# Optimization experiments

Measured on AMD Instinct MI355X. Metric: run time of the kernel, lower is better.

Reference implementation:

```python
import jax, jax.numpy as jnp
import numpy as np

K = 5        # spline kernel_size per dim (dim=2 -> 25 kernel weights)
NPG = 75     # MNIST superpixel nodes per graph


def _spline_conv(x, src, dst, pseudo, emask, W, root, bias):
    """SplineConv, dim=2, kernel_size=5, degree=1 open splines, aggr='mean'.
    emask in {0,1} masks out coalesced-away (duplicate/self-loop) edges."""
    n = x.shape[0]
    v = jnp.clip(pseudo, 0.0, 1.0) * (K - 1)
    bot = jnp.clip(jnp.floor(v), 0, K - 2)
    frac = v - bot                                   # [E,2]
    bot = bot.astype(jnp.int32)
    xj = x[src] * emask[:, None]                     # [E,Fin] gathered source feats
    # aggregate-then-transform: acc[k,i,:] = sum over edges into i with basis k
    acc = jnp.zeros((K * K, n, x.shape[1]), x.dtype)
    for o0 in (0, 1):
        for o1 in (0, 1):
            w = (frac[:, 0] if o0 else 1.0 - frac[:, 0]) * (frac[:, 1] if o1 else 1.0 - frac[:, 1])
            kk = (bot[:, 0] + o0) + K * (bot[:, 1] + o1)
            acc = acc.at[kk, dst].add(w[:, None] * xj)
    out = jnp.einsum('knf,kfo->no', acc, W)
    deg = jax.ops.segment_sum(emask, dst, num_segments=n)
    return out / jnp.maximum(deg, 1.0)[:, None] + x @ root + bias


def _pool(x, pos, valid, batch, src, dst, emask, size, G, B):
    """voxel_grid + max_pool with static shapes: S=B*G*G clusters, masked."""
    S = B * G * G
    c = jnp.clip(jnp.floor(pos / size).astype(jnp.int32), 0, G - 1)
    cl = batch * (G * G) + c[:, 1] * G + c[:, 0]
    xm = jnp.where(valid[:, None] > 0, x, -1e30)
    px = jax.ops.segment_max(xm, cl, num_segments=S)
    cnt = jax.ops.segment_sum(valid, cl, num_segments=S)
    sval = (cnt > 0).astype(x.dtype)
    px = jnp.where(sval[:, None] > 0, px, 0.0)
    ppos = jax.ops.segment_sum(pos * valid[:, None], cl, num_segments=S) / jnp.maximum(cnt, 1.0)[:, None]
    nb = jnp.arange(S, dtype=jnp.int32) // (G * G)
    # remap edges to clusters; mask self loops and duplicates (= coalesce)
    nsrc, ndst = cl[src], cl[dst]
    m = (emask > 0) & (nsrc != ndst)
    a0 = jnp.where(m, nsrc, S)
    b0 = jnp.where(m, ndst, S)
    order = jnp.lexsort((b0, a0))
    a, b = a0[order], b0[order]
    first = jnp.concatenate([jnp.array([True]), (a[1:] != a[:-1]) | (b[1:] != b[:-1])])
    keep = jnp.zeros(src.shape[0], dtype=bool).at[order].set(first & (a < S))
    kf = keep.astype(x.dtype)
    # T.Cartesian(cat=False, norm=True): pseudo = (pos_src-pos_dst)/(2*max|.|)+0.5
    cart = ppos[nsrc] - ppos[ndst]
    amax = jnp.maximum(jnp.max(jnp.abs(cart) * kf[:, None]), 1e-12)
    pseudo = cart / (2.0 * amax) + 0.5
    return px, ppos, sval, nb, nsrc, ndst, kf, pseudo


def _forward(x, pos, src, dst, W1, r1, b1, W2, r2, b2, W3, r3, b3, fw1, fb1, fw2, fb2):
    N = x.shape[0]
    B = N // NPG
    batch = jnp.arange(N, dtype=jnp.int32) // NPG
    valid = jnp.ones((N,), x.dtype)
    emask = jnp.ones((src.shape[0],), x.dtype)
    cart = pos[src] - pos[dst]
    pseudo = cart / (2.0 * jnp.maximum(jnp.max(jnp.abs(cart)), 1e-12)) + 0.5
    x = jax.nn.elu(_spline_conv(x, src, dst, pseudo, emask, W1, r1, b1))
    x, pos, valid, batch, src, dst, emask, pseudo = _pool(x, pos, valid, batch, src, dst, emask, 5.0, 6, B)
    x = jax.nn.elu(_spline_conv(x, src, dst, pseudo, emask, W2, r2, b2))
    x, pos, valid, batch, src, dst, emask, pseudo = _pool(x, pos, valid, batch, src, dst, emask, 7.0, 5, B)
    x = jax.nn.elu(_spline_conv(x, src, dst, pseudo, emask, W3, r3, b3))
    # max_pool_x(cluster, x, batch, size=4): 2x2 voxel grid (size=14, end=27.99)
    c = jnp.clip(jnp.floor(pos / 14.0).astype(jnp.int32), 0, 1)
    cl = batch * 4 + c[:, 1] * 2 + c[:, 0]
    xm = jnp.where(valid[:, None] > 0, x, -1e30)
    px = jax.ops.segment_max(xm, cl, num_segments=B * 4)
    cnt = jax.ops.segment_sum(valid, cl, num_segments=B * 4)
    px = jnp.where((cnt > 0)[:, None], px, 0.0)
    h = jax.nn.elu(px.reshape(B, 4 * 64) @ fw1.T + fb1)
    logits = h @ fw2.T + fb2  # F.dropout is identity in eval mode
    return jax.nn.log_softmax(logits, axis=1)


def setup_inputs() -> dict:
    key = jax.random.key(0)
    ks = jax.random.split(key, 16)
    B, EPG = 1024, 1392
    N = B * NPG
    x = jax.random.normal(ks[0], (N, 1), jnp.float32)
    pos = jax.random.uniform(ks[1], (N, 2), jnp.float32) * 27.99
    s = jax.random.randint(ks[2], (B, EPG), 0, NPG)
    d = (s + 1 + jax.random.randint(ks[3], (B, EPG), 0, NPG - 1)) % NPG  # no self loops
    off = (jnp.arange(B, dtype=jnp.int32) * NPG)[:, None]
    src = (s + off).reshape(-1)
    dst = (d + off).reshape(-1)
    rn = lambda k, sh, sc: jax.random.normal(k, sh, jnp.float32) * sc
    return dict(x=x, pos=pos, src=src, dst=dst,
                W1=rn(ks[4], (25, 1, 32), 0.2), r1=rn(ks[5], (1, 32), 0.2), b1=jnp.zeros((32,), jnp.float32),
                W2=rn(ks[6], (25, 32, 64), 0.05), r2=rn(ks[7], (32, 64), 0.1), b2=jnp.zeros((64,), jnp.float32),
                W3=rn(ks[8], (25, 64, 64), 0.04), r3=rn(ks[9], (64, 64), 0.08), b3=jnp.zeros((64,), jnp.float32),
                fw1=rn(ks[10], (128, 256), 0.06), fb1=jnp.zeros((128,), jnp.float32),
                fw2=rn(ks[11], (10, 128), 0.09), fb2=jnp.zeros((10,), jnp.float32))


def reference(x, pos, src, dst, W1, r1, b1, W2, r2, b2, W3, r3, b3, fw1, fb1, fw2, fb2):
    return _forward(x, pos, src, dst, W1, r1, b1, W2, r2, b2, W3, r3, b3, fw1, fb1, fw2, fb2)
```

## Files before the change

### kernel.cpp

```cpp
#include <hip/hip_runtime.h>
#include <math.h>

#define NPG 75
#define KDIM 5

typedef _Float16 half8 __attribute__((ext_vector_type(8)));
typedef _Float16 half4 __attribute__((ext_vector_type(4)));
typedef float f32x4 __attribute__((ext_vector_type(4)));

__device__ __forceinline__ float eluf(float v){ return v > 0.f ? v : expf(v) - 1.f; }

__device__ __forceinline__ void atomAddF(float* p, float v){ unsafeAtomicAdd(p, v); }

__device__ __forceinline__ unsigned fenc(float f){
    unsigned u = __float_as_uint(f);
    return (u & 0x80000000u) ? ~u : (u | 0x80000000u);
}
__device__ __forceinline__ float fdec(unsigned u){
    return (u & 0x80000000u) ? __uint_as_float(u & 0x7FFFFFFFu) : __uint_as_float(~u);
}

__device__ __forceinline__ void fma25(float (&r)[25], const float (&wx)[5], const float (&wyx)[5]){
    #pragma unroll
    for (int b1 = 0; b1 < 5; b1++)
        #pragma unroll
        for (int b0 = 0; b0 < 5; b0++)
            asm("v_fmac_f32 %0, %1, %2" : "+v"(r[b1 * 5 + b0]) : "v"(wx[b0]), "v"(wyx[b1]));
}

__device__ __forceinline__ void spline2(float c0, float c1, float am, int* kks, float* wsp){
    float denom = 2.f * fmaxf(am, 1e-12f);
    float p0 = c0 / denom + 0.5f;
    float p1 = c1 / denom + 0.5f;
    p0 = fminf(fmaxf(p0, 0.f), 1.f) * 4.f;
    p1 = fminf(fmaxf(p1, 0.f), 1.f) * 4.f;
    float b0 = fminf(floorf(p0), 3.f);
    float b1 = fminf(floorf(p1), 3.f);
    float f0 = p0 - b0, f1 = p1 - b1;
    int i0 = (int)b0, i1 = (int)b1;
    wsp[0] = (1.f - f0) * (1.f - f1); kks[0] = i0     + KDIM *  i1;
    wsp[1] =        f0  * (1.f - f1); kks[1] = i0 + 1 + KDIM *  i1;
    wsp[2] = (1.f - f0) *        f1 ; kks[2] = i0     + KDIM * (i1 + 1);
    wsp[3] =        f0  *        f1 ; kks[3] = i0 + 1 + KDIM * (i1 + 1);
}

__global__ __launch_bounds__(256) void amax0_k(
        const float* __restrict__ pos, const int* __restrict__ src,
        const int* __restrict__ dst, int E4, unsigned* __restrict__ outbits){
    float cand = 0.f;
    for (int i = blockIdx.x * 256 + threadIdx.x; i < E4; i += gridDim.x * 256){
        int4 s4 = ((const int4*)src)[i];
        int4 d4 = ((const int4*)dst)[i];
        #pragma unroll
        for (int k = 0; k < 4; k++){
            int s = (&s4.x)[k], d = (&d4.x)[k];
            float c0 = pos[s*2]   - pos[d*2];
            float c1 = pos[s*2+1] - pos[d*2+1];
            cand = fmaxf(cand, fmaxf(fabsf(c0), fabsf(c1)));
        }
    }
    __shared__ float sm[256];
    sm[threadIdx.x] = cand; __syncthreads();
    for (int o = 128; o > 0; o >>= 1){
        if (threadIdx.x < o) sm[threadIdx.x] = fmaxf(sm[threadIdx.x], sm[threadIdx.x + o]);
        __syncthreads();
    }
    if (threadIdx.x == 0) atomicMax(outbits, __float_as_uint(sm[0]));
}

__global__ __launch_bounds__(512) void conv1pool1_k(
        const float* __restrict__ x, const float* __restrict__ pos,
        const int* __restrict__ src, const int* __restrict__ dst, int EPG,
        const unsigned* __restrict__ amaxp,
        const float* __restrict__ W1, const float* __restrict__ r1, const float* __restrict__ b1,
        float* __restrict__ px1, float* __restrict__ pp1, float* __restrict__ sv1,
        int* __restrict__ cl1){
    __shared__ __align__(16) float acc[NPG * 28];
    __shared__ float deg[NPG];
    __shared__ float xl[NPG], p0l[NPG], p1l[NPG];
    __shared__ int   cli[NPG];
    __shared__ float W1s[800], r1s[32], b1s[32];
    __shared__ unsigned px[36 * 32];
    __shared__ float cnt[36], ps[72];

    const int b = blockIdx.x, t = threadIdx.x;
    const int n0 = b * NPG, e0 = b * EPG;

    const float am = __uint_as_float(*amaxp);

    for (int i = t; i < NPG * 28; i += 512) acc[i] = 0.f;
    for (int i = t; i < 36 * 32; i += 512) px[i] = 0u;
    if (t < NPG) deg[t] = 0.f;
    if (t < 36) cnt[t] = 0.f;
    if (t < 72) ps[t] = 0.f;
    for (int i = t; i < 800; i += 512) W1s[i] = W1[i];
    if (t < 32){ r1s[t] = r1[t]; b1s[t] = b1[t]; }
    if (t < NPG){
        float p0 = pos[(n0 + t) * 2], p1 = pos[(n0 + t) * 2 + 1];
        xl[t] = x[n0 + t]; p0l[t] = p0; p1l[t] = p1;
        int c0 = min(max((int)floorf(p0 / 5.f), 0), 5);
        int c1 = min(max((int)floorf(p1 / 5.f), 0), 5);
        int c = c1 * 6 + c0;
        cli[t] = c;
        cl1[n0 + t] = b * 36 + c;
    }
    __syncthreads();

    const int o = t & 31;
    float wreg[25];
    #pragma unroll
    for (int k = 0; k < 25; k++) wreg[k] = W1s[k * 32 + o];
    const float rro = r1s[o], bbo = b1s[o];

    if (t < NPG){
        int c = cli[t];
        atomAddF(&cnt[c], 1.f);
        atomAddF(&ps[c*2],     p0l[t]);
        atomAddF(&ps[c*2 + 1], p1l[t]);
    }

    for (int e = t; e < EPG; e += 512){
        int s = src[e0 + e] - n0;
        int d = dst[e0 + e] - n0;
        float c0 = p0l[s] - p0l[d];
        float c1 = p1l[s] - p1l[d];
        int kks[4]; float wsp[4];
        spline2(c0, c1, am, kks, wsp);
        float xv = xl[s];
        #pragma unroll
        for (int c = 0; c < 4; c++) atomAddF(&acc[d*28 + kks[c]], wsp[c] * xv);
        atomAddF(&deg[d], 1.f);
    }
    __syncthreads();

    const int ii = t >> 5;
    #pragma unroll
    for (int r = 0; r < 5; r++){
        int i = ii + r * 16;
        if (i < NPG){
            const float4* ar = (const float4*)(acc + i * 28);
            float s = 0.f;
            #pragma unroll
            for (int q = 0; q < 7; q++){
                float4 aq = ar[q];
                s += aq.x * wreg[q*4];
                if (q*4 + 1 < 25) s += aq.y * wreg[q*4 + 1];
                if (q*4 + 2 < 25) s += aq.z * wreg[q*4 + 2];
                if (q*4 + 3 < 25) s += aq.w * wreg[q*4 + 3];
            }
            float v = s / fmaxf(deg[i], 1.f) + xl[i] * rro + bbo;
            v = eluf(v);
            atomicMax(&px[cli[i]*32 + o], fenc(v));
        }
    }
    __syncthreads();

    for (int idx = t; idx < 36 * 32; idx += 512){
        int s_ = idx >> 5;
        px1[(size_t)(b*36)*32 + idx] = (cnt[s_] > 0.f) ? fdec(px[idx]) : 0.f;
    }
    if (t < 36){
        float c = cnt[t], m = fmaxf(c, 1.f);
        pp1[(b*36 + t)*2]     = ps[t*2] / m;
        pp1[(b*36 + t)*2 + 1] = ps[t*2 + 1] / m;
        sv1[b*36 + t] = (c > 0.f) ? 1.f : 0.f;
    }
}

template<int GG, int NN>
__global__ __launch_bounds__(1024) void dedup_csr_k(
        const int* src_in, const int* dst_in,
        const int* __restrict__ clmap, const unsigned char* __restrict__ kf_in,
        unsigned char* kf_out, int* es_out, int* ed_out,
        const float* __restrict__ pp, int EPG,
        int* __restrict__ easrc, float2* __restrict__ ecart,
        int* __restrict__ rowptr2, int* __restrict__ kcnt, unsigned* __restrict__ amaxbits){
    __shared__ unsigned pm[GG * GG];
    __shared__ float degs[GG];
    __shared__ int rs[GG + 1];
    __shared__ int cur[GG];
    __shared__ float red[16];
    __shared__ int   clS[NN];
    __shared__ float ppS[2 * GG];

    const int b = blockIdx.x, t = threadIdx.x;
    const int lane = t & 63, wid = t >> 6;
    const int e0 = b * EPG;
    const int cbase = b * GG;

    for (int i = t; i < GG * GG; i += 1024) pm[i] = 0xFFFFFFFFu;
    if (t < GG) degs[t] = 0.f;
    if (t < NN) clS[t] = clmap[b * NN + t] - cbase;
    if (t < 2 * GG) ppS[t] = pp[cbase * 2 + t];
    __syncthreads();

    const int niter = (EPG + 1023) / 1024;
    int la[2], lb[2]; bool lm[2];
    const int nbase = b * NN;
    for (int it = 0; it < niter; it++){
        int e = t + it * 1024;
        lm[it] = false;
        if (e < EPG){
            int a  = clS[src_in[e0 + e] - nbase];
            int bb = clS[dst_in[e0 + e] - nbase];
            la[it] = a; lb[it] = bb;
            es_out[e0 + e] = cbase + a; ed_out[e0 + e] = cbase + bb;
            bool m = (kf_in ? (kf_in[e0 + e] != 0) : true) && (a != bb);
            lm[it] = m;
            if (m) atomicMin(&pm[a * GG + bb], (unsigned)e);
        }
    }
    __syncthreads();

    float cand = 0.f;
    bool kept[2]; float lc0[2], lc1[2];
    for (int it = 0; it < niter; it++){
        int e = t + it * 1024;
        kept[it] = false;
        if (e < EPG){
            bool k = false;
            if (lm[it]) k = (pm[la[it] * GG + lb[it]] == (unsigned)e);
            kept[it] = k;
            if (kf_out) kf_out[e0 + e] = k ? 1 : 0;
            if (k){
                atomAddF(&degs[lb[it]], 1.f);
                float c0 = ppS[la[it]*2]     - ppS[lb[it]*2];
                float c1 = ppS[la[it]*2 + 1] - ppS[lb[it]*2 + 1];
                lc0[it] = c0; lc1[it] = c1;
                cand = fmaxf(cand, fmaxf(fabsf(c0), fabsf(c1)));
            }
        }
    }
    #pragma unroll
    for (int o = 1; o < 64; o <<= 1) cand = fmaxf(cand, __shfl_xor(cand, o, 64));
    if (lane == 0) red[wid] = cand;
    __syncthreads();
    if (t == 0){
        float m = red[0];
        #pragma unroll
        for (int i = 1; i < 16; i++) m = fmaxf(m, red[i]);
        atomicMax(amaxbits, __float_as_uint(m));
    }
    if (t < 64){
        int v = (t < GG) ? (int)degs[t] : 0;
        int incl = v;
        #pragma unroll
        for (int o = 1; o < 64; o <<= 1){
            int u = __shfl_up(incl, o, 64);
            if (t >= o) incl += u;
        }
        if (t == 0) rs[0] = 0;
        if (t < GG) rs[t + 1] = incl;
    }
    __syncthreads();
    if (t < GG){
        rowptr2[(cbase + t)*2]     = e0 + rs[t];
        rowptr2[(cbase + t)*2 + 1] = e0 + rs[t + 1];
        cur[t] = rs[t];
    }
    if (t == 0) kcnt[b] = rs[GG];
    __syncthreads();
    for (int it = 0; it < niter; it++){
        if (kept[it]){
            int slot = atomicAdd(&cur[lb[it]], 1);
            easrc[e0 + slot] = cbase + la[it];
            ecart[e0 + slot] = make_float2(lc0[it], lc1[it]);
        }
    }
}

__global__ __launch_bounds__(1024) void dedup_pool_k(
        const int* __restrict__ src_in, const int* __restrict__ dst_in,
        const unsigned char* __restrict__ kf_in,
        const float* __restrict__ xin,
        const float* __restrict__ pp1, const float* __restrict__ sv1,
        int EPG,
        float* __restrict__ px2, float* __restrict__ pp2, float* __restrict__ sv2,
        int* __restrict__ easrc, float2* __restrict__ ecart,
        int* __restrict__ rowptr2, int* __restrict__ kcnt, unsigned* __restrict__ amaxbits){
    constexpr int GG = 25, NN = 36;
    __shared__ unsigned pm[GG * GG];
    __shared__ float degs[GG];
    __shared__ int rs[GG + 1];
    __shared__ int cur[GG];
    __shared__ float red[16];
    __shared__ int   clS[NN];
    __shared__ int   vld[NN];
    __shared__ float ppS[2 * GG];
    __shared__ unsigned px[GG * 64];
    __shared__ float cnt[GG], ps[2 * GG];

    const int b = blockIdx.x, t = threadIdx.x;
    const int lane = t & 63, wid = t >> 6;
    const int e0 = b * EPG;
    const int cbase = b * GG;
    const int nb36  = b * NN;

    for (int i = t; i < GG * GG; i += 1024) pm[i] = 0xFFFFFFFFu;
    for (int i = t; i < GG * 64; i += 1024) px[i] = 0u;
    if (t < GG){ degs[t] = 0.f; cnt[t] = 0.f; }
    if (t < 2 * GG) ps[t] = 0.f;
    if (t < NN){
        float v  = sv1[nb36 + t];
        float p0 = pp1[(nb36 + t)*2], p1 = pp1[(nb36 + t)*2 + 1];
        int c0 = min(max((int)floorf(p0 / 7.f), 0), 4);
        int c1 = min(max((int)floorf(p1 / 7.f), 0), 4);
        clS[t] = c1 * 5 + c0;
        vld[t] = (v > 0.f) ? 1 : 0;
    }
    __syncthreads();

    if (t < NN && vld[t]){
        int c = clS[t];
        atomAddF(&cnt[c], 1.f);
        atomAddF(&ps[c*2],     pp1[(nb36 + t)*2]);
        atomAddF(&ps[c*2 + 1], pp1[(nb36 + t)*2 + 1]);
    }
    for (int idx = t; idx < NN * 64; idx += 1024){
        int i = idx >> 6, f = idx & 63;
        if (vld[i])
            atomicMax(&px[clS[i]*64 + f], fenc(xin[(size_t)(nb36 + i)*64 + f]));
    }
    const int niter = (EPG + 1023) / 1024;
    int la[2], lb[2]; bool lm[2];
    for (int it = 0; it < niter; it++){
        int e = t + it * 1024;
        lm[it] = false;
        if (e < EPG){
            int a  = clS[src_in[e0 + e] - nb36];
            int bb = clS[dst_in[e0 + e] - nb36];
            la[it] = a; lb[it] = bb;
            bool m = (kf_in[e0 + e] != 0) && (a != bb);
            lm[it] = m;
            if (m) atomicMin(&pm[a * GG + bb], (unsigned)e);
        }
    }
    __syncthreads();

    if (t < GG){
        float c = cnt[t], m = fmaxf(c, 1.f);
        float q0 = ps[t*2] / m, q1 = ps[t*2 + 1] / m;
        ppS[t*2] = q0; ppS[t*2 + 1] = q1;
        pp2[(cbase + t)*2]     = q0;
        pp2[(cbase + t)*2 + 1] = q1;
        sv2[cbase + t] = (c > 0.f) ? 1.f : 0.f;
    }
    for (int idx = t; idx < GG * 64; idx += 1024){
        int s_ = idx >> 6;
        px2[(size_t)cbase*64 + idx] = (cnt[s_] > 0.f) ? fdec(px[idx]) : 0.f;
    }
    __syncthreads();

    float cand = 0.f;
    bool kept[2]; float lc0[2], lc1[2];
    for (int it = 0; it < niter; it++){
        int e = t + it * 1024;
        kept[it] = false;
        if (e < EPG){
            bool k = false;
            if (lm[it]) k = (pm[la[it] * GG + lb[it]] == (unsigned)e);
            kept[it] = k;
            if (k){
                atomAddF(&degs[lb[it]], 1.f);
                float c0 = ppS[la[it]*2]     - ppS[lb[it]*2];
                float c1 = ppS[la[it]*2 + 1] - ppS[lb[it]*2 + 1];
                lc0[it] = c0; lc1[it] = c1;
                cand = fmaxf(cand, fmaxf(fabsf(c0), fabsf(c1)));
            }
        }
    }
    #pragma unroll
    for (int o = 1; o < 64; o <<= 1) cand = fmaxf(cand, __shfl_xor(cand, o, 64));
    if (lane == 0) red[wid] = cand;
    __syncthreads();
    if (t == 0){
        float m = red[0];
        #pragma unroll
        for (int i = 1; i < 16; i++) m = fmaxf(m, red[i]);
        atomicMax(amaxbits, __float_as_uint(m));
    }
    if (t < 64){
        int v = (t < GG) ? (int)degs[t] : 0;
        int incl = v;
        #pragma unroll
        for (int o = 1; o < 64; o <<= 1){
            int u = __shfl_up(incl, o, 64);
            if (t >= o) incl += u;
        }
        if (t == 0) rs[0] = 0;
        if (t < GG) rs[t + 1] = incl;
    }
    __syncthreads();
    if (t < GG){
        rowptr2[(cbase + t)*2]     = e0 + rs[t];
        rowptr2[(cbase + t)*2 + 1] = e0 + rs[t + 1];
        cur[t] = rs[t];
    }
    if (t == 0) kcnt[b] = rs[GG];
    __syncthreads();
    for (int it = 0; it < niter; it++){
        if (kept[it]){
            int slot = atomicAdd(&cur[lb[it]], 1);
            easrc[e0 + slot] = cbase + la[it];
            ecart[e0 + slot] = make_float2(lc0[it], lc1[it]);
        }
    }
}

__global__ void espline_k(const float2* __restrict__ ecart, const unsigned* __restrict__ amaxp,
                          const int* __restrict__ kcnt, int EPG, int E,
                          float* __restrict__ edata){
    int i = blockIdx.x * 256 + threadIdx.x;
    if (i >= E) return;
    int b = i / EPG;
    if (i - b * EPG >= kcnt[b]) return;
    float2 c = ecart[i];
    float am = __uint_as_float(*amaxp);
    float denom = 2.f * fmaxf(am, 1e-12f);
    float p0 = fminf(fmaxf(c.x / denom + 0.5f, 0.f), 1.f) * 4.f;
    float p1 = fminf(fmaxf(c.y / denom + 0.5f, 0.f), 1.f) * 4.f;
    float b0 = fminf(floorf(p0), 3.f);
    float b1 = fminf(floorf(p1), 3.f);
    int i0 = (int)b0, i1 = (int)b1;
    float f0 = p0 - b0, f1 = p1 - b1;
    float wx[5], wy[5];
    #pragma unroll
    for (int k = 0; k < 5; k++){
        wx[k] = (k == i0) ? (1.f - f0) : ((k == i0 + 1) ? f0 : 0.f);
        wy[k] = (k == i1) ? (1.f - f1) : ((k == i1 + 1) ? f1 : 0.f);
    }
    float* d = edata + (size_t)i * 8;
    *(float4*)(d)     = make_float4(wx[0], wx[1], wx[2], wx[3]);
    *(float4*)(d + 4) = make_float4(wy[0], wy[1], wy[2], wy[3]);
}

__global__ void wswz2_k(const float* __restrict__ W2, const float* __restrict__ r2,
                        const float* __restrict__ W3, const float* __restrict__ r3,
                        _Float16* __restrict__ Wz2, _Float16* __restrict__ Wz3){
    int gid = blockIdx.x * 256 + threadIdx.x;
    const int T2 = 26 * 32 * 64;
    const int T3 = 26 * 64 * 64;
    const float* W; const float* root; _Float16* Wz; int FIN; int g;
    if (gid < T2){ W = W2; root = r2; Wz = Wz2; FIN = 32; g = gid; }
    else if (gid < T2 + T3){ W = W3; root = r3; Wz = Wz3; FIN = 64; g = gid - T2; }
    else return;
    int k = g >> 6, n = g & 63;
    float v = (k < 25 * FIN) ? W[(size_t)k * 64 + n] : root[(size_t)(k - 25 * FIN) * 64 + n];
    int kt = k >> 5, kr = k & 31, quad = kr >> 3, j = kr & 7;
    int lane = (quad << 4) | (n & 15);
    int nt = n >> 4;
    Wz[(((size_t)(kt * 4 + nt) * 64 + lane) << 3) + j] = (_Float16)v;
}

template<int FIN>
__global__ __launch_bounds__(256) void conv_gather_k(
        const float* __restrict__ x, const int* __restrict__ easrc,
        const float* __restrict__ edata,
        const int* __restrict__ rowptr2, _Float16* __restrict__ Aout){
    constexpr int KTOT = 26 * FIN;
    const int lane = threadIdx.x & 63;
    const int node = blockIdx.x * 4 + (threadIdx.x >> 6);
    const int row0 = rowptr2[node*2], row1 = rowptr2[node*2 + 1];
    constexpr int STEP = (FIN == 32) ? 2 : 1;
    const int sub = (FIN == 32) ? (lane >> 5) : 0;
    const int f = lane & (FIN - 1);

    float r[25];
    #pragma unroll
    for (int b = 0; b < 25; b++) r[b] = 0.f;

    int iCur = row0 + sub;
    int aNext = 0;
    float4 waC, wbC;
    float xvCur = 0.f;
    if (iCur < row1){
        int aCur = easrc[iCur];
        const float* d = edata + (size_t)iCur * 8;
        waC = *(const float4*)(d); wbC = *(const float4*)(d + 4);
        xvCur = x[(size_t)aCur * FIN + f];
        int i1 = (iCur + STEP < row1) ? iCur + STEP : iCur;
        aNext = easrc[i1];
    }
    for (; iCur < row1; iCur += STEP){
        int iN  = iCur + STEP;
        int iNs = (iN < row1) ? iN : iCur;
        int iN2 = (iN + STEP < row1) ? iN + STEP : iNs;
        const float* dn = edata + (size_t)iNs * 8;
        float4 waN = *(const float4*)(dn);
        float4 wbN = *(const float4*)(dn + 4);
        float xvN = x[(size_t)aNext * FIN + f];
        int aN2 = easrc[iN2];
        float wx4 = 1.f - (waC.x + waC.y + waC.z + waC.w);
        float wy4 = 1.f - (wbC.x + wbC.y + wbC.z + wbC.w);
        float wx[5]  = {waC.x, waC.y, waC.z, waC.w, wx4};
        float wyx[5] = {wbC.x * xvCur, wbC.y * xvCur, wbC.z * xvCur, wbC.w * xvCur, wy4 * xvCur};
        fma25(r, wx, wyx);
        waC = waN; wbC = wbN; xvCur = xvN; aNext = aN2;
    }

    if (FIN == 32){
        #pragma unroll
        for (int b = 0; b < 25; b++) r[b] += __shfl_xor(r[b], 32, 64);
    }

    float inv = 1.f / (float)max(row1 - row0, 1);
    _Float16* dstrow = Aout + (size_t)node * KTOT;
    if (FIN == 64){
        #pragma unroll
        for (int b = 0; b < 25; b++) dstrow[b * 64 + f] = (_Float16)(r[b] * inv);
        dstrow[25 * 64 + f] = (_Float16)x[(size_t)node * 64 + f];
    } else {
        #pragma unroll
        for (int b = 0; b < 25; b++)
            if ((b & 1) == sub) dstrow[b * 32 + f] = (_Float16)(r[b] * inv);
        if (sub == 0) dstrow[25 * 32 + f] = (_Float16)x[(size_t)node * 32 + f];
    }
}

template<int KTOT>
__global__ __launch_bounds__(256) void conv_mfma_k(
        const _Float16* __restrict__ A, const _Float16* __restrict__ Wz,
        const float* __restrict__ bias, int M, float* __restrict__ out){
    constexpr int NSTEP = KTOT / 32;
    const int w = threadIdx.x >> 6, lane = threadIdx.x & 63;
    const int m0 = blockIdx.x * 64 + w * 16;
    const int quad = lane >> 4;

    f32x4 acc[4];
    #pragma unroll
    for (int nt = 0; nt < 4; nt++) acc[nt] = (f32x4){0.f, 0.f, 0.f, 0.f};

    const half8* __restrict__ Arow = (const half8*)(A + (size_t)(m0 + (lane & 15)) * KTOT);
    const half8* __restrict__ Wp   = (const half8*)Wz + lane;

    for (int kt = 0; kt < NSTEP; kt++){
        half8 a = Arow[kt * 4 + quad];
        #pragma unroll
        for (int nt = 0; nt < 4; nt++){
            half8 b = Wp[(kt * 4 + nt) * 64];
            acc[nt] = __builtin_amdgcn_mfma_f32_16x16x32_f16(a, b, acc[nt], 0, 0, 0);
        }
    }

    float* cp = out + (size_t)m0 * 64;
    const int r = quad * 4, c = lane & 15;
    #pragma unroll
    for (int nt = 0; nt < 4; nt++){
        float bv = bias[nt * 16 + c];
        #pragma unroll
        for (int i = 0; i < 4; i++)
            cp[(size_t)(r + i) * 64 + nt * 16 + c] = eluf(acc[nt][i] + bv);
    }
}

__global__ __launch_bounds__(256) void final_k(
        const float* __restrict__ xin, const float* __restrict__ ppin,
        const float* __restrict__ svin,
        const float* __restrict__ fw1, const float* __restrict__ fb1,
        const float* __restrict__ fw2, const float* __restrict__ fb2,
        float* __restrict__ out){
    __shared__ unsigned px[4 * 64];
    __shared__ float cnt[4];
    __shared__ int cli[25];
    __shared__ float xr[256];
    __shared__ float h[128];
    __shared__ float lg[10];
    __shared__ float lse;
    const int b = blockIdx.x, t = threadIdx.x;

    if (t < 4*64) px[t] = 0u;
    if (t < 4) cnt[t] = 0.f;
    if (t < 25){
        float v  = svin[b*25 + t];
        float p0 = ppin[(b*25 + t)*2], p1 = ppin[(b*25 + t)*2 + 1];
        int c0 = min(max((int)floorf(p0 / 14.f), 0), 1);
        int c1 = min(max((int)floorf(p1 / 14.f), 0), 1);
        int c = c1 * 2 + c0;
        cli[t] = (v > 0.f) ? c : -1;
    }
    __syncthreads();
    if (t < 25 && cli[t] >= 0) atomAddF(&cnt[cli[t]], 1.f);
    __syncthreads();
    for (int idx = t; idx < 25 * 64; idx += 256){
        int i = idx >> 6, f = idx & 63;
        if (cli[i] >= 0)
            atomicMax(&px[cli[i]*64 + f], fenc(xin[(size_t)(b*25 + i)*64 + f]));
    }
    __syncthreads();
    xr[t] = (cnt[t >> 6] > 0.f) ? fdec(px[t]) : 0.f;
    __syncthreads();
    if (t < 128){
        float s = fb1[t];
        const float4* wrow = (const float4*)(fw1 + (size_t)t * 256);
        #pragma unroll 4
        for (int i = 0; i < 64; i++){
            float4 q = wrow[i];
            s += xr[i*4]   * q.x;
            s += xr[i*4+1] * q.y;
            s += xr[i*4+2] * q.z;
            s += xr[i*4+3] * q.w;
        }
        h[t] = eluf(s);
    }
    __syncthreads();
    if (t < 10){
        float s2 = fb2[t];
        const float* w2 = fw2 + (size_t)t * 128;
        for (int j = 0; j < 128; j++) s2 += h[j] * w2[j];
        lg[t] = s2;
    }
    __syncthreads();
    if (t == 0){
        float m = lg[0];
        for (int c = 1; c < 10; c++) m = fmaxf(m, lg[c]);
        float se = 0.f;
        for (int c = 0; c < 10; c++) se += expf(lg[c] - m);
        lse = m + logf(se);
    }
    __syncthreads();
    if (t < 10) out[(size_t)b*10 + t] = lg[t] - lse;
}

extern "C" void kernel_launch(void* const* d_in, const int* in_sizes, int n_in,
                              void* d_out, int out_size, void* d_ws, size_t ws_size,
                              hipStream_t stream) {
    const float* x   = (const float*)d_in[0];
    const float* pos = (const float*)d_in[1];
    const int*   src = (const int*)d_in[2];
    const int*   dst = (const int*)d_in[3];
    const float* W1  = (const float*)d_in[4];
    const float* r1  = (const float*)d_in[5];
    const float* b1  = (const float*)d_in[6];
    const float* W2  = (const float*)d_in[7];
    const float* r2  = (const float*)d_in[8];
    const float* b2  = (const float*)d_in[9];
    const float* W3  = (const float*)d_in[10];
    const float* r3  = (const float*)d_in[11];
    const float* b3  = (const float*)d_in[12];
    const float* fw1 = (const float*)d_in[13];
    const float* fb1 = (const float*)d_in[14];
    const float* fw2 = (const float*)d_in[15];
    const float* fb2 = (const float*)d_in[16];
    float* out = (float*)d_out;

    const int N   = in_sizes[0];
    const int E   = in_sizes[2];
    const int B   = N / NPG;
    const int EPG = E / B;
    const int S1  = B * 36;
    const int S2  = B * 25;

    float* w = (float*)d_ws;
    size_t off = 0;
    auto alloc = [&](size_t nelem){ size_t o = off; off += (nelem + 63) & ~(size_t)63; return o; };

    size_t o_scal = alloc(4);
    size_t o_px1  = alloc((size_t)S1 * 32);
    size_t o_pp1  = alloc((size_t)S1 * 2);
    size_t o_sv1  = alloc(S1);
    size_t o_cl1  = alloc(N);
    size_t o_kf1  = alloc((E + 3) / 4);
    size_t o_es1  = alloc(E);
    size_t o_ed1  = alloc(E);
    size_t o_easrc= alloc(E);
    size_t o_ecart= alloc((size_t)2 * E);
    size_t o_edat = alloc((size_t)8 * E);
    size_t o_kcnt = alloc(B);
    size_t o_rp2  = alloc((size_t)2 * S1);
    size_t o_rp3  = alloc((size_t)2 * S2);
    size_t o_out2 = alloc((size_t)S1 * 64);
    size_t o_px2  = alloc((size_t)S2 * 64);
    size_t o_pp2  = alloc((size_t)S2 * 2);
    size_t o_sv2  = alloc(S2);
    size_t o_out3 = alloc((size_t)S2 * 64);
    size_t o_wz2  = alloc((size_t)26 * 32 * 64 / 2 + 64);
    size_t o_wz3  = alloc((size_t)26 * 64 * 64 / 2 + 64);
    size_t accAhalfs = (size_t)S1 * 832 > (size_t)S2 * 1664 ? (size_t)S1 * 832 : (size_t)S2 * 1664;
    size_t o_accA = alloc((accAhalfs + 1) / 2);

    hipMemsetAsync(w + o_scal, 0, 4 * sizeof(float), stream);

    unsigned* scal = (unsigned*)(w + o_scal);
    _Float16* Wz2  = (_Float16*)(w + o_wz2);
    _Float16* Wz3  = (_Float16*)(w + o_wz3);
    _Float16* A16  = (_Float16*)(w + o_accA);
    auto nb = [](long long t){ return (unsigned)((t + 255) / 256); };

    wswz2_k<<<nb(26 * 32 * 64 + 26 * 64 * 64), 256, 0, stream>>>(W2, r2, W3, r3, Wz2, Wz3);

    const int E4 = E / 4;
    int gA = (E4 + 255) / 256; if (gA > 512) gA = 512;
    amax0_k<<<gA, 256, 0, stream>>>(pos, src, dst, E4, scal + 0);
    conv1pool1_k<<<B, 512, 0, stream>>>(x, pos, src, dst, EPG, scal + 0, W1, r1, b1,
                                        w + o_px1, w + o_pp1, w + o_sv1, (int*)(w + o_cl1));

    dedup_csr_k<36, NPG><<<B, 1024, 0, stream>>>(
        src, dst, (int*)(w + o_cl1), nullptr,
        (unsigned char*)(w + o_kf1), (int*)(w + o_es1), (int*)(w + o_ed1),
        w + o_pp1, EPG, (int*)(w + o_easrc), (float2*)(w + o_ecart),
        (int*)(w + o_rp2), (int*)(w + o_kcnt), scal + 1);
    espline_k<<<nb(E), 256, 0, stream>>>((float2*)(w + o_ecart), scal + 1,
                                         (int*)(w + o_kcnt), EPG, E, w + o_edat);

    conv_gather_k<32><<<S1 / 4, 256, 0, stream>>>(
        w + o_px1, (int*)(w + o_easrc), w + o_edat,
        (int*)(w + o_rp2), A16);
    conv_mfma_k<832><<<S1 / 64, 256, 0, stream>>>(A16, Wz2, b2, S1, w + o_out2);

    dedup_pool_k<<<B, 1024, 0, stream>>>(
        (int*)(w + o_es1), (int*)(w + o_ed1), (unsigned char*)(w + o_kf1),
        w + o_out2, w + o_pp1, w + o_sv1, EPG,
        w + o_px2, w + o_pp2, w + o_sv2,
        (int*)(w + o_easrc), (float2*)(w + o_ecart),
        (int*)(w + o_rp3), (int*)(w + o_kcnt), scal + 2);
    espline_k<<<nb(E), 256, 0, stream>>>((float2*)(w + o_ecart), scal + 2,
                                         (int*)(w + o_kcnt), EPG, E, w + o_edat);

    conv_gather_k<64><<<S2 / 4, 256, 0, stream>>>(
        w + o_px2, (int*)(w + o_easrc), w + o_edat,
        (int*)(w + o_rp3), A16);
    conv_mfma_k<1664><<<S2 / 64, 256, 0, stream>>>(A16, Wz3, b3, S2, w + o_out3);

    final_k<<<B, 256, 0, stream>>>(w + o_out3, w + o_pp2, w + o_sv2,
                                   fw1, fb1, fw2, fb2, out);
}
```

Baseline: 360.0 us.

## Fuse conv1+pool1 with level-1 edge dedup and drive pool2 from the CSR

The separate dedup_csr kernel is merged into the conv1/pool1 kernel. Per-graph edge endpoints are packed into shared memory, and the cluster-pair dedup, degree count and CSR build happen in the same block, so the cl1/kf1/es1/ed1 global buffers are gone. The second-level dedup now reads the already deduplicated level-1 CSR (easrc plus rowptr) instead of re-scanning all original edges with keep flags. This saves a launch and global traffic but adds shared memory use and a linear row search per edge. It also reads and writes easrc in the same kernel, which risks a race, and it hard-codes EPG at most 2048.

```diff
diff --git a/kernel.cpp b/kernel.cpp
--- a/kernel.cpp
+++ b/kernel.cpp
@@ -68,30 +68,38 @@
     if (threadIdx.x == 0) atomicMax(outbits, __float_as_uint(sm[0]));
 }
 
-__global__ __launch_bounds__(512) void conv1pool1_k(
+__global__ __launch_bounds__(512) void conv1dedup_k(
         const float* __restrict__ x, const float* __restrict__ pos,
         const int* __restrict__ src, const int* __restrict__ dst, int EPG,
         const unsigned* __restrict__ amaxp,
         const float* __restrict__ W1, const float* __restrict__ r1, const float* __restrict__ b1,
         float* __restrict__ px1, float* __restrict__ pp1, float* __restrict__ sv1,
-        int* __restrict__ cl1){
+        int* __restrict__ easrc, float2* __restrict__ ecart,
+        int* __restrict__ rowptr2, int* __restrict__ kcnt, unsigned* __restrict__ amaxbits){
     __shared__ __align__(16) float acc[NPG * 28];
     __shared__ float deg[NPG];
     __shared__ float xl[NPG], p0l[NPG], p1l[NPG];
     __shared__ int   cli[NPG];
     __shared__ float W1s[800], r1s[32], b1s[32];
     __shared__ unsigned px[36 * 32];
-    __shared__ float cnt[36], ps[72];
+    __shared__ float cnt[36], ps[72], ppS[72];
+    __shared__ unsigned pm[36 * 36];
+    __shared__ float degs[36];
+    __shared__ int rs[37], cur[36];
+    __shared__ float red[8];
+    __shared__ unsigned short sdS[2048];
 
     const int b = blockIdx.x, t = threadIdx.x;
+    const int lane = t & 63, wid = t >> 6;
     const int n0 = b * NPG, e0 = b * EPG;
 
     const float am = __uint_as_float(*amaxp);
 
     for (int i = t; i < NPG * 28; i += 512) acc[i] = 0.f;
     for (int i = t; i < 36 * 32; i += 512) px[i] = 0u;
+    for (int i = t; i < 36 * 36; i += 512) pm[i] = 0xFFFFFFFFu;
     if (t < NPG) deg[t] = 0.f;
-    if (t < 36) cnt[t] = 0.f;
+    if (t < 36){ cnt[t] = 0.f; degs[t] = 0.f; }
     if (t < 72) ps[t] = 0.f;
     for (int i = t; i < 800; i += 512) W1s[i] = W1[i];
     if (t < 32){ r1s[t] = r1[t]; b1s[t] = b1[t]; }
@@ -100,17 +108,9 @@
         xl[t] = x[n0 + t]; p0l[t] = p0; p1l[t] = p1;
         int c0 = min(max((int)floorf(p0 / 5.f), 0), 5);
         int c1 = min(max((int)floorf(p1 / 5.f), 0), 5);
-        int c = c1 * 6 + c0;
-        cli[t] = c;
-        cl1[n0 + t] = b * 36 + c;
-    }
-    __syncthreads();
-
-    const int o = t & 31;
-    float wreg[25];
-    #pragma unroll
-    for (int k = 0; k < 25; k++) wreg[k] = W1s[k * 32 + o];
-    const float rro = r1s[o], bbo = b1s[o];
+        cli[t] = c1 * 6 + c0;
+    }
+    __syncthreads();
 
     if (t < NPG){
         int c = cli[t];
@@ -118,39 +118,71 @@
         atomAddF(&ps[c*2],     p0l[t]);
         atomAddF(&ps[c*2 + 1], p1l[t]);
     }
-
-    for (int e = t; e < EPG; e += 512){
-        int s = src[e0 + e] - n0;
-        int d = dst[e0 + e] - n0;
-        float c0 = p0l[s] - p0l[d];
-        float c1 = p1l[s] - p1l[d];
-        int kks[4]; float wsp[4];
-        spline2(c0, c1, am, kks, wsp);
-        float xv = xl[s];
-        #pragma unroll
-        for (int c = 0; c < 4; c++) atomAddF(&acc[d*28 + kks[c]], wsp[c] * xv);
-        atomAddF(&deg[d], 1.f);
-    }
-    __syncthreads();
-
-    const int ii = t >> 5;
-    #pragma unroll
-    for (int r = 0; r < 5; r++){
-        int i = ii + r * 16;
-        if (i < NPG){
-            const float4* ar = (const float4*)(acc + i * 28);
-            float s = 0.f;
+    #pragma unroll 4
+    for (int it = 0; it < 4; it++){
+        int e = t + it * 512;
+        if (e < EPG){
+            int s = src[e0 + e] - n0;
+            int d = dst[e0 + e] - n0;
+            sdS[e] = (unsigned short)(s | (d << 8));
+            float c0 = p0l[s] - p0l[d];
+            float c1 = p1l[s] - p1l[d];
+            int kks[4]; float wsp[4];
+            spline2(c0, c1, am, kks, wsp);
+            float xv = xl[s];
             #pragma unroll
-            for (int q = 0; q < 7; q++){
-                float4 aq = ar[q];
-                s += aq.x * wreg[q*4];
-                if (q*4 + 1 < 25) s += aq.y * wreg[q*4 + 1];
-                if (q*4 + 2 < 25) s += aq.z * wreg[q*4 + 2];
-                if (q*4 + 3 < 25) s += aq.w * wreg[q*4 + 3];
+            for (int c = 0; c < 4; c++) atomAddF(&acc[d*28 + kks[c]], wsp[c] * xv);
+            atomAddF(&deg[d], 1.f);
+        }
+    }
+    __syncthreads();
+
+    if (t < 36){
+        float c = cnt[t], m = fmaxf(c, 1.f);
+        float q0 = ps[t*2] / m, q1 = ps[t*2 + 1] / m;
+        ppS[t*2] = q0; ppS[t*2 + 1] = q1;
+        pp1[(b*36 + t)*2]     = q0;
+        pp1[(b*36 + t)*2 + 1] = q1;
+        sv1[b*36 + t] = (c > 0.f) ? 1.f : 0.f;
+    }
+    {
+        const int o = t & 31;
+        float wreg[25];
+        #pragma unroll
+        for (int k = 0; k < 25; k++) wreg[k] = W1s[k * 32 + o];
+        const float rro = r1s[o], bbo = b1s[o];
+        const int ii = t >> 5;
+        #pragma unroll
+        for (int r = 0; r < 5; r++){
+            int i = ii + r * 16;
+            if (i < NPG){
+                const float4* ar = (const float4*)(acc + i * 28);
+                float s = 0.f;
+                #pragma unroll
+                for (int q = 0; q < 7; q++){
+                    float4 aq = ar[q];
+                    s += aq.x * wreg[q*4];
+                    if (q*4 + 1 < 25) s += aq.y * wreg[q*4 + 1];
+                    if (q*4 + 2 < 25) s += aq.z * wreg[q*4 + 2];
+                    if (q*4 + 3 < 25) s += aq.w * wreg[q*4 + 3];
+                }
+                float v = s / fmaxf(deg[i], 1.f) + xl[i] * rro + bbo;
+                v = eluf(v);
+                atomicMax(&px[cli[i]*32 + o], fenc(v));
             }
-            float v = s / fmaxf(deg[i], 1.f) + xl[i] * rro + bbo;
-            v = eluf(v);
-            atomicMax(&px[cli[i]*32 + o], fenc(v));
+        }
+    }
+    int lab[4];
+    #pragma unroll 4
+    for (int it = 0; it < 4; it++){
+        int e = t + it * 512;
+        lab[it] = 0;
+        if (e < EPG){
+            int sd = (int)sdS[e];
+            int a  = cli[sd & 255];
+            int bb = cli[sd >> 8];
+            lab[it] = a | (bb << 8) | ((a != bb) ? 0x10000 : 0);
+            if (a != bb) atomicMin(&pm[a * 36 + bb], (unsigned)e);
         }
     }
     __syncthreads();
@@ -159,74 +191,19 @@
         int s_ = idx >> 5;
         px1[(size_t)(b*36)*32 + idx] = (cnt[s_] > 0.f) ? fdec(px[idx]) : 0.f;
     }
-    if (t < 36){
-        float c = cnt[t], m = fmaxf(c, 1.f);
-        pp1[(b*36 + t)*2]     = ps[t*2] / m;
-        pp1[(b*36 + t)*2 + 1] = ps[t*2 + 1] / m;
-        sv1[b*36 + t] = (c > 0.f) ? 1.f : 0.f;
-    }
-}
-
-template<int GG, int NN>
-__global__ __launch_bounds__(1024) void dedup_csr_k(
-        const int* src_in, const int* dst_in,
-        const int* __restrict__ clmap, const unsigned char* __restrict__ kf_in,
-        unsigned char* kf_out, int* es_out, int* ed_out,
-        const float* __restrict__ pp, int EPG,
-        int* __restrict__ easrc, float2* __restrict__ ecart,
-        int* __restrict__ rowptr2, int* __restrict__ kcnt, unsigned* __restrict__ amaxbits){
-    __shared__ unsigned pm[GG * GG];
-    __shared__ float degs[GG];
-    __shared__ int rs[GG + 1];
-    __shared__ int cur[GG];
-    __shared__ float red[16];
-    __shared__ int   clS[NN];
-    __shared__ float ppS[2 * GG];
-
-    const int b = blockIdx.x, t = threadIdx.x;
-    const int lane = t & 63, wid = t >> 6;
-    const int e0 = b * EPG;
-    const int cbase = b * GG;
-
-    for (int i = t; i < GG * GG; i += 1024) pm[i] = 0xFFFFFFFFu;
-    if (t < GG) degs[t] = 0.f;
-    if (t < NN) clS[t] = clmap[b * NN + t] - cbase;
-    if (t < 2 * GG) ppS[t] = pp[cbase * 2 + t];
-    __syncthreads();
-
-    const int niter = (EPG + 1023) / 1024;
-    int la[2], lb[2]; bool lm[2];
-    const int nbase = b * NN;
-    for (int it = 0; it < niter; it++){
-        int e = t + it * 1024;
-        lm[it] = false;
-        if (e < EPG){
-            int a  = clS[src_in[e0 + e] - nbase];
-            int bb = clS[dst_in[e0 + e] - nbase];
-            la[it] = a; lb[it] = bb;
-            es_out[e0 + e] = cbase + a; ed_out[e0 + e] = cbase + bb;
-            bool m = (kf_in ? (kf_in[e0 + e] != 0) : true) && (a != bb);
-            lm[it] = m;
-            if (m) atomicMin(&pm[a * GG + bb], (unsigned)e);
-        }
-    }
-    __syncthreads();
-
     float cand = 0.f;
-    bool kept[2]; float lc0[2], lc1[2];
-    for (int it = 0; it < niter; it++){
-        int e = t + it * 1024;
-        kept[it] = false;
-        if (e < EPG){
-            bool k = false;
-            if (lm[it]) k = (pm[la[it] * GG + lb[it]] == (unsigned)e);
-            kept[it] = k;
-            if (kf_out) kf_out[e0 + e] = k ? 1 : 0;
-            if (k){
-                atomAddF(&degs[lb[it]], 1.f);
-                float c0 = ppS[la[it]*2]     - ppS[lb[it]*2];
-                float c1 = ppS[la[it]*2 + 1] - ppS[lb[it]*2 + 1];
-                lc0[it] = c0; lc1[it] = c1;
+    unsigned keptM = 0;
+    #pragma unroll 4
+    for (int it = 0; it < 4; it++){
+        int e = t + it * 512;
+        int L = lab[it];
+        if (L & 0x10000){
+            int a = L & 255, bb = (L >> 8) & 255;
+            if (pm[a * 36 + bb] == (unsigned)e){
+                keptM |= 1u << it;
+                atomAddF(&degs[bb], 1.f);
+                float c0 = ppS[a*2]     - ppS[bb*2];
+                float c1 = ppS[a*2 + 1] - ppS[bb*2 + 1];
                 cand = fmaxf(cand, fmaxf(fabsf(c0), fabsf(c1)));
             }
         }
@@ -238,11 +215,11 @@
     if (t == 0){
         float m = red[0];
         #pragma unroll
-        for (int i = 1; i < 16; i++) m = fmaxf(m, red[i]);
+        for (int i = 1; i < 8; i++) m = fmaxf(m, red[i]);
         atomicMax(amaxbits, __float_as_uint(m));
     }
     if (t < 64){
-        int v = (t < GG) ? (int)degs[t] : 0;
+        int v = (t < 36) ? (int)degs[t] : 0;
         int incl = v;
         #pragma unroll
         for (int o = 1; o < 64; o <<= 1){
@@ -250,28 +227,31 @@
             if (t >= o) incl += u;
         }
         if (t == 0) rs[0] = 0;
-        if (t < GG) rs[t + 1] = incl;
-    }
-    __syncthreads();
-    if (t < GG){
-        rowptr2[(cbase + t)*2]     = e0 + rs[t];
-        rowptr2[(cbase + t)*2 + 1] = e0 + rs[t + 1];
+        if (t < 36) rs[t + 1] = incl;
+    }
+    __syncthreads();
+    if (t < 36){
+        rowptr2[(b*36 + t)*2]     = e0 + rs[t];
+        rowptr2[(b*36 + t)*2 + 1] = e0 + rs[t + 1];
         cur[t] = rs[t];
     }
-    if (t == 0) kcnt[b] = rs[GG];
-    __syncthreads();
-    for (int it = 0; it < niter; it++){
-        if (kept[it]){
-            int slot = atomicAdd(&cur[lb[it]], 1);
-            easrc[e0 + slot] = cbase + la[it];
-            ecart[e0 + slot] = make_float2(lc0[it], lc1[it]);
+    if (t == 0) kcnt[b] = rs[36];
+    __syncthreads();
+    #pragma unroll 4
+    for (int it = 0; it < 4; it++){
+        if (keptM & (1u << it)){
+            int L = lab[it];
+            int a = L & 255, bb = (L >> 8) & 255;
+            int slot = atomicAdd(&cur[bb], 1);
+            easrc[e0 + slot] = b*36 + a;
+            ecart[e0 + slot] = make_float2(ppS[a*2] - ppS[bb*2], ppS[a*2 + 1] - ppS[bb*2 + 1]);
         }
     }
 }
 
 __global__ __launch_bounds__(1024) void dedup_pool_k(
-        const int* __restrict__ src_in, const int* __restrict__ dst_in,
-        const unsigned char* __restrict__ kf_in,
+        const int* __restrict__ easrc_in, const int* __restrict__ rowptr_in,
+        const int* __restrict__ kcnt_in,
         const float* __restrict__ xin,
         const float* __restrict__ pp1, const float* __restrict__ sv1,
         int EPG,
@@ -286,15 +266,17 @@
     __shared__ float red[16];
     __shared__ int   clS[NN];
     __shared__ int   vld[NN];
+    __shared__ int   rsS[NN + 1];
     __shared__ float ppS[2 * GG];
     __shared__ unsigned px[GG * 64];
     __shared__ float cnt[GG], ps[2 * GG];
+    __shared__ unsigned short abS[1280];
 
     const int b = blockIdx.x, t = threadIdx.x;
     const int lane = t & 63, wid = t >> 6;
     const int e0 = b * EPG;
-    const int cbase = b * GG;
-    const int nb36  = b * NN;
+    const int cb25 = b * GG;
+    const int nb36 = b * NN;
 
     for (int i = t; i < GG * GG; i += 1024) pm[i] = 0xFFFFFFFFu;
     for (int i = t; i < GG * 64; i += 1024) px[i] = 0u;
@@ -307,8 +289,12 @@
         int c1 = min(max((int)floorf(p1 / 7.f), 0), 4);
         clS[t] = c1 * 5 + c0;
         vld[t] = (v > 0.f) ? 1 : 0;
-    }
-    __syncthreads();
+        rsS[t] = rowptr_in[(nb36 + t)*2] - e0;
+    }
+    if (t == 0) rsS[NN] = kcnt_in[b];
+    __syncthreads();
+
+    const int kn = rsS[NN];
 
     if (t < NN && vld[t]){
         int c = clS[t];
@@ -321,18 +307,16 @@
         if (vld[i])
             atomicMax(&px[clS[i]*64 + f], fenc(xin[(size_t)(nb36 + i)*64 + f]));
     }
-    const int niter = (EPG + 1023) / 1024;
-    int la[2], lb[2]; bool lm[2];
-    for (int it = 0; it < niter; it++){
-        int e = t + it * 1024;
-        lm[it] = false;
-        if (e < EPG){
-            int a  = clS[src_in[e0 + e] - nb36];
-            int bb = clS[dst_in[e0 + e] - nb36];
-            la[it] = a; lb[it] = bb;
-            bool m = (kf_in[e0 + e] != 0) && (a != bb);
-            lm[it] = m;
-            if (m) atomicMin(&pm[a * GG + bb], (unsigned)e);
+    #pragma unroll 2
+    for (int it = 0; it < 2; it++){
+        int s = t + it * 1024;
+        if (s < kn){
+            int r = 0;
+            while (r < NN - 1 && rsS[r + 1] <= s) r++;
+            int a2 = clS[easrc_in[e0 + s] - nb36];
+            int b2 = clS[r];
+            abS[s] = (unsigned short)(a2 | (b2 << 8) | ((a2 != b2) ? 0x8000 : 0));
+            if (a2 != b2) atomicMin(&pm[a2 * GG + b2], (unsigned)s);
         }
     }
     __syncthreads();
@@ -341,31 +325,30 @@
         float c = cnt[t], m = fmaxf(c, 1.f);
         float q0 = ps[t*2] / m, q1 = ps[t*2 + 1] / m;
         ppS[t*2] = q0; ppS[t*2 + 1] = q1;
-        pp2[(cbase + t)*2]     = q0;
-        pp2[(cbase + t)*2 + 1] = q1;
-        sv2[cbase + t] = (c > 0.f) ? 1.f : 0.f;
+        pp2[(cb25 + t)*2]     = q0;
+        pp2[(cb25 + t)*2 + 1] = q1;
+        sv2[cb25 + t] = (c > 0.f) ? 1.f : 0.f;
     }
     for (int idx = t; idx < GG * 64; idx += 1024){
         int s_ = idx >> 6;
-        px2[(size_t)cbase*64 + idx] = (cnt[s_] > 0.f) ? fdec(px[idx]) : 0.f;
+        px2[(size_t)cb25*64 + idx] = (cnt[s_] > 0.f) ? fdec(px[idx]) : 0.f;
     }
     __syncthreads();
 
     float cand = 0.f;
-    bool kept[2]; float lc0[2], lc1[2];
-    for (int it = 0; it < niter; it++){
-        int e = t + it * 1024;
-        kept[it] = false;
-        if (e < EPG){
-            bool k = false;
-            if (lm[it]) k = (pm[la[it] * GG + lb[it]] == (unsigned)e);
-            kept[it] = k;
-            if (k){
-                atomAddF(&degs[lb[it]], 1.f);
-                float c0 = ppS[la[it]*2]     - ppS[lb[it]*2];
-                float c1 = ppS[la[it]*2 + 1] - ppS[lb[it]*2 + 1];
-                lc0[it] = c0; lc1[it] = c1;
-                cand = fmaxf(cand, fmaxf(fabsf(c0), fabsf(c1)));
+    #pragma unroll 2
+    for (int it = 0; it < 2; it++){
+        int s = t + it * 1024;
+        if (s < kn){
+            int A = (int)abS[s];
+            if (A & 0x8000){
+                int a2 = A & 255, b2 = (A >> 8) & 127;
+                if (pm[a2 * GG + b2] == (unsigned)s){
+                    atomAddF(&degs[b2], 1.f);
+                    float c0 = ppS[a2*2]     - ppS[b2*2];
+                    float c1 = ppS[a2*2 + 1] - ppS[b2*2 + 1];
+                    cand = fmaxf(cand, fmaxf(fabsf(c0), fabsf(c1)));
+                }
             }
         }
     }
@@ -392,17 +375,25 @@
     }
     __syncthreads();
     if (t < GG){
-        rowptr2[(cbase + t)*2]     = e0 + rs[t];
-        rowptr2[(cbase + t)*2 + 1] = e0 + rs[t + 1];
+        rowptr2[(cb25 + t)*2]     = e0 + rs[t];
+        rowptr2[(cb25 + t)*2 + 1] = e0 + rs[t + 1];
         cur[t] = rs[t];
     }
     if (t == 0) kcnt[b] = rs[GG];
     __syncthreads();
-    for (int it = 0; it < niter; it++){
-        if (kept[it]){
-            int slot = atomicAdd(&cur[lb[it]], 1);
-            easrc[e0 + slot] = cbase + la[it];
-            ecart[e0 + slot] = make_float2(lc0[it], lc1[it]);
+    #pragma unroll 2
+    for (int it = 0; it < 2; it++){
+        int s = t + it * 1024;
+        if (s < kn){
+            int A = (int)abS[s];
+            if (A & 0x8000){
+                int a2 = A & 255, b2 = (A >> 8) & 127;
+                if (pm[a2 * GG + b2] == (unsigned)s){
+                    int slot = atomicAdd(&cur[b2], 1);
+                    easrc[e0 + slot] = cb25 + a2;
+                    ecart[e0 + slot] = make_float2(ppS[a2*2] - ppS[b2*2], ppS[a2*2 + 1] - ppS[b2*2 + 1]);
+                }
+            }
         }
     }
 }
@@ -658,10 +649,6 @@
     size_t o_px1  = alloc((size_t)S1 * 32);
     size_t o_pp1  = alloc((size_t)S1 * 2);
     size_t o_sv1  = alloc(S1);
-    size_t o_cl1  = alloc(N);
-    size_t o_kf1  = alloc((E + 3) / 4);
-    size_t o_es1  = alloc(E);
-    size_t o_ed1  = alloc(E);
     size_t o_easrc= alloc(E);
     size_t o_ecart= alloc((size_t)2 * E);
     size_t o_edat = alloc((size_t)8 * E);
@@ -691,14 +678,11 @@
     const int E4 = E / 4;
     int gA = (E4 + 255) / 256; if (gA > 512) gA = 512;
     amax0_k<<<gA, 256, 0, stream>>>(pos, src, dst, E4, scal + 0);
-    conv1pool1_k<<<B, 512, 0, stream>>>(x, pos, src, dst, EPG, scal + 0, W1, r1, b1,
-                                        w + o_px1, w + o_pp1, w + o_sv1, (int*)(w + o_cl1));
-
-    dedup_csr_k<36, NPG><<<B, 1024, 0, stream>>>(
-        src, dst, (int*)(w + o_cl1), nullptr,
-        (unsigned char*)(w + o_kf1), (int*)(w + o_es1), (int*)(w + o_ed1),
-        w + o_pp1, EPG, (int*)(w + o_easrc), (float2*)(w + o_ecart),
-        (int*)(w + o_rp2), (int*)(w + o_kcnt), scal + 1);
+
+    conv1dedup_k<<<B, 512, 0, stream>>>(x, pos, src, dst, EPG, scal + 0, W1, r1, b1,
+                                        w + o_px1, w + o_pp1, w + o_sv1,
+                                        (int*)(w + o_easrc), (float2*)(w + o_ecart),
+                                        (int*)(w + o_rp2), (int*)(w + o_kcnt), scal + 1);
     espline_k<<<nb(E), 256, 0, stream>>>((float2*)(w + o_ecart), scal + 1,
                                          (int*)(w + o_kcnt), EPG, E, w + o_edat);
 
@@ -708,7 +692,7 @@
     conv_mfma_k<832><<<S1 / 64, 256, 0, stream>>>(A16, Wz2, b2, S1, w + o_out2);
 
     dedup_pool_k<<<B, 1024, 0, stream>>>(
-        (int*)(w + o_es1), (int*)(w + o_ed1), (unsigned char*)(w + o_kf1),
+        (int*)(w + o_easrc), (int*)(w + o_rp2), (int*)(w + o_kcnt),
         w + o_out2, w + o_pp1, w + o_sv1, EPG,
         w + o_px2, w + o_pp2, w + o_sv2,
         (int*)(w + o_easrc), (float2*)(w + o_ecart),
```

Result: faster. 338.8 us (-5.9%).
